# Kernel optimization log

Measured on AMD Instinct MI355X. Metric: run time of the kernel, lower is better.

## Reference

```python
import jax, jax.numpy as jnp
import numpy as np

B, N, DIM = 8, 1024, 1024
HEADS, DIM_HEAD = 16, 64
INNER = HEADS * DIM_HEAD  # 1024


def setup_inputs() -> dict:
    key = jax.random.key(0)
    k1, k2, k3 = jax.random.split(key, 3)
    x = jax.random.normal(k1, (B, N, DIM), dtype=jnp.float32)
    # Dense kernels (Glorot-ish scale for numerical sanity)
    w_qkv = jax.random.normal(k2, (DIM, 3 * INNER), dtype=jnp.float32) * (DIM ** -0.5)
    w_out = jax.random.normal(k3, (INNER, DIM), dtype=jnp.float32) * (INNER ** -0.5)
    b_out = jnp.zeros((DIM,), dtype=jnp.float32)
    return {"x": x, "w_qkv": w_qkv, "w_out": w_out, "b_out": b_out}


def reference(x, w_qkv, w_out, b_out):
    scale = DIM_HEAD ** -0.5
    qkv = x @ w_qkv                                   # [B, N, 3*INNER]
    q, k, v = jnp.split(qkv, 3, axis=-1)              # each [B, N, INNER]

    def to_heads(t):
        # [B, N, H*Dh] -> [B, H, N, Dh]
        return t.reshape(B, N, HEADS, DIM_HEAD).transpose(0, 2, 1, 3)

    q, k, v = to_heads(q), to_heads(k), to_heads(v)
    dots = jnp.einsum("bhid,bhjd->bhij", q, k) * scale   # [B, H, N, N]
    attn = jax.nn.softmax(dots, axis=-1)
    out = jnp.einsum("bhij,bhjd->bhid", attn, v)          # [B, H, N, Dh]
    out = out.transpose(0, 2, 1, 3).reshape(B, N, INNER)  # merge heads
    return out @ w_out + b_out                            # project_out (dropout inactive at inference)
```

## Files before the change

kernel.cpp:

```cpp
#include <hip/hip_runtime.h>
#include <hip/hip_bf16.h>
#include <math.h>

typedef __bf16 bf16_t;
typedef __bf16 bf16x4 __attribute__((ext_vector_type(4)));
typedef __bf16 bf16x8 __attribute__((ext_vector_type(8)));
typedef float f32x4 __attribute__((ext_vector_type(4)));

#define LOG2E 1.44269504088896340736f

__global__ __launch_bounds__(256) void transpose_f32_bf16(const float* __restrict__ in,
                                                          bf16_t* __restrict__ out,
                                                          int R, int C) {
  __shared__ bf16_t t[64][65];
  const int c0 = blockIdx.x * 64, r0 = blockIdx.y * 64;
  const int tx = threadIdx.x, ty = threadIdx.y;
#pragma unroll
  for (int i = 0; i < 16; i++) {
    int r = ty + i * 4;
    t[r][tx] = (bf16_t)in[(size_t)(r0 + r) * C + c0 + tx];
  }
  __syncthreads();
#pragma unroll
  for (int i = 0; i < 16; i++) {
    int r = ty + i * 4;
    out[(size_t)(c0 + r) * R + r0 + tx] = t[tx][r];
  }
}

template <int MODE>
__global__ __launch_bounds__(256) void gemm128(const float* __restrict__ Af,
                                               const bf16_t* __restrict__ Ab,
                                               const bf16_t* __restrict__ Bt,
                                               bf16_t* __restrict__ Qb,
                                               bf16_t* __restrict__ Kb,
                                               bf16_t* __restrict__ Vtb,
                                               const float* __restrict__ bias,
                                               float* __restrict__ Out) {
  constexpr int K = 1024;
  __shared__ __align__(16) bf16_t As[128 * 72];
  __shared__ __align__(16) bf16_t Bs[128 * 72];
  const int m0 = blockIdx.y * 128, n0 = blockIdx.x * 128;
  const int tid = threadIdx.x;
  const int w = tid >> 6, l = tid & 63;
  const int lr = l & 15, lq = l >> 4;
  const int wm = (w & 1) * 64, wn = (w >> 1) * 64;
  f32x4 acc[4][4] = {};

  for (int k0 = 0; k0 < K; k0 += 64) {
    if (MODE == 0) {
#pragma unroll
      for (int i = 0; i < 8; i++) {
        int c = tid + i * 256;
        int r = c >> 4, kc = c & 15;
        f32x4 a = *(const f32x4*)&Af[(size_t)(m0 + r) * K + k0 + kc * 4];
        bf16x4 v;
        v[0] = (bf16_t)a[0]; v[1] = (bf16_t)a[1];
        v[2] = (bf16_t)a[2]; v[3] = (bf16_t)a[3];
        *(bf16x4*)&As[r * 72 + kc * 4] = v;
      }
    } else {
#pragma unroll
      for (int i = 0; i < 4; i++) {
        int c = tid + i * 256;
        int r = c >> 3, kc = c & 7;
        *(bf16x8*)&As[r * 72 + kc * 8] =
            *(const bf16x8*)&Ab[(size_t)(m0 + r) * K + k0 + kc * 8];
      }
    }
#pragma unroll
    for (int i = 0; i < 4; i++) {
      int c = tid + i * 256;
      int r = c >> 3, kc = c & 7;
      *(bf16x8*)&Bs[r * 72 + kc * 8] =
          *(const bf16x8*)&Bt[(size_t)(n0 + r) * K + k0 + kc * 8];
    }
    __syncthreads();
#pragma unroll
    for (int ks = 0; ks < 2; ks++) {
      bf16x8 af[4], bfr[4];
#pragma unroll
      for (int mt = 0; mt < 4; mt++)
        af[mt] = *(const bf16x8*)&As[(wm + mt * 16 + lr) * 72 + ks * 32 + lq * 8];
#pragma unroll
      for (int nt = 0; nt < 4; nt++)
        bfr[nt] = *(const bf16x8*)&Bs[(wn + nt * 16 + lr) * 72 + ks * 32 + lq * 8];
#pragma unroll
      for (int mt = 0; mt < 4; mt++)
#pragma unroll
        for (int nt = 0; nt < 4; nt++)
          acc[mt][nt] = __builtin_amdgcn_mfma_f32_16x16x32_bf16(af[mt], bfr[nt],
                                                                acc[mt][nt], 0, 0, 0);
    }
    __syncthreads();
  }

#pragma unroll
  for (int mt = 0; mt < 4; mt++)
#pragma unroll
    for (int nt = 0; nt < 4; nt++)
#pragma unroll
      for (int i = 0; i < 4; i++) {
        int m = m0 + wm + mt * 16 + lq * 4 + i;
        int c = n0 + wn + nt * 16 + lr;
        float v = acc[mt][nt][i];
        if (MODE == 1) {
          Out[(size_t)m * 1024 + c] = v + bias[c];
        } else {
          int b = m >> 10, n = m & 1023;
          int which = c >> 10, cc = c & 1023;
          int hh = cc >> 6, d = cc & 63;
          size_t qk = ((size_t)((b * 16 + hh) * 1024 + n)) * 64 + d;
          if (which == 0)
            Qb[qk] = (bf16_t)(v * (0.125f * LOG2E));
          else if (which == 1)
            Kb[qk] = (bf16_t)v;
          else
            Vtb[((size_t)((b * 16 + hh) * 64 + d)) * 1024 + n] = (bf16_t)v;
        }
      }
}

#define KVS 68
#define PS  72
__global__ __launch_bounds__(256) void attn128(const bf16_t* __restrict__ Qb,
                                               const bf16_t* __restrict__ Kb,
                                               const bf16_t* __restrict__ Vtb,
                                               bf16_t* __restrict__ Ob) {
  __shared__ __align__(16) bf16_t Ks[2][64 * KVS];
  __shared__ __align__(16) bf16_t Vs[2][64 * KVS];
  __shared__ __align__(16) bf16_t Pl[4 * 32 * PS];
  const int bid = blockIdx.x;
  const int qt = bid & 7, h = (bid >> 3) & 15, b = bid >> 7;
  const bf16_t* Qh = Qb + (size_t)((b * 16 + h) * 1024) * 64;
  const bf16_t* Kh = Kb + (size_t)((b * 16 + h) * 1024) * 64;
  const bf16_t* Vh = Vtb + (size_t)((b * 16 + h) * 64) * 1024;
  const int tid = threadIdx.x, w = tid >> 6, l = tid & 63;
  const int lr = l & 15, lq = l >> 4;
  const int q0 = qt * 128 + w * 32;

  bf16x8 onesf;
#pragma unroll
  for (int i = 0; i < 8; i++) onesf[i] = (lr == 0) ? (bf16_t)1.0f : (bf16_t)0.0f;

  const int sr = tid >> 3, sc = tid & 7;

  bf16x8 qf[2][2];
#pragma unroll
  for (int mt = 0; mt < 2; mt++)
#pragma unroll
    for (int ks = 0; ks < 2; ks++)
      qf[mt][ks] = *(const bf16x8*)&Qh[(size_t)(q0 + mt * 16 + lr) * 64 + ks * 32 + lq * 8];

  {
    bf16x8 k0 = *(const bf16x8*)&Kh[(size_t)sr * 64 + sc * 8];
    bf16x8 k1 = *(const bf16x8*)&Kh[(size_t)(sr + 32) * 64 + sc * 8];
    bf16x8 v0 = *(const bf16x8*)&Vh[(size_t)sr * 1024 + sc * 8];
    bf16x8 v1 = *(const bf16x8*)&Vh[(size_t)(sr + 32) * 1024 + sc * 8];
    *(bf16x8*)&Ks[0][sr * KVS + sc * 8] = k0;
    *(bf16x8*)&Ks[0][(sr + 32) * KVS + sc * 8] = k1;
    *(bf16x8*)&Vs[0][sr * KVS + sc * 8] = v0;
    *(bf16x8*)&Vs[0][(sr + 32) * KVS + sc * 8] = v1;
  }
  __syncthreads();

  f32x4 o[2][4] = {};
  f32x4 o5[2] = {};
  bf16_t* pw = &Pl[w * 32 * PS];

  for (int it = 0; it < 16; ++it) {
    const int buf = it & 1;
    bf16x8 nk0, nk1, nv0, nv1;
    if (it < 15) {
      const int jn = (it + 1) * 64;
      nk0 = *(const bf16x8*)&Kh[(size_t)(jn + sr) * 64 + sc * 8];
      nk1 = *(const bf16x8*)&Kh[(size_t)(jn + sr + 32) * 64 + sc * 8];
      nv0 = *(const bf16x8*)&Vh[(size_t)sr * 1024 + jn + sc * 8];
      nv1 = *(const bf16x8*)&Vh[(size_t)(sr + 32) * 1024 + jn + sc * 8];
    }
    f32x4 s[2][4] = {};
#pragma unroll
    for (int ks = 0; ks < 2; ks++)
#pragma unroll
      for (int nt = 0; nt < 4; nt++) {
        bf16x8 kf = *(const bf16x8*)&Ks[buf][(nt * 16 + lr) * KVS + ks * 32 + lq * 8];
#pragma unroll
        for (int mt = 0; mt < 2; mt++)
          s[mt][nt] = __builtin_amdgcn_mfma_f32_16x16x32_bf16(qf[mt][ks], kf, s[mt][nt], 0, 0, 0);
      }
#pragma unroll
    for (int mt = 0; mt < 2; mt++)
#pragma unroll
      for (int nt = 0; nt < 4; nt++)
#pragma unroll
        for (int i = 0; i < 4; i++)
          pw[(mt * 16 + lq * 4 + i) * PS + nt * 16 + lr] = (bf16_t)exp2f(s[mt][nt][i]);
#pragma unroll
    for (int ks = 0; ks < 2; ks++) {
      bf16x8 af[2];
#pragma unroll
      for (int mt = 0; mt < 2; mt++)
        af[mt] = *(const bf16x8*)&pw[(mt * 16 + lr) * PS + ks * 32 + lq * 8];
#pragma unroll
      for (int nt = 0; nt < 4; nt++) {
        bf16x8 vf = *(const bf16x8*)&Vs[buf][(nt * 16 + lr) * KVS + ks * 32 + lq * 8];
#pragma unroll
        for (int mt = 0; mt < 2; mt++)
          o[mt][nt] = __builtin_amdgcn_mfma_f32_16x16x32_bf16(af[mt], vf, o[mt][nt], 0, 0, 0);
      }
#pragma unroll
      for (int mt = 0; mt < 2; mt++)
        o5[mt] = __builtin_amdgcn_mfma_f32_16x16x32_bf16(af[mt], onesf, o5[mt], 0, 0, 0);
    }
    if (it < 15) {
      *(bf16x8*)&Ks[buf ^ 1][sr * KVS + sc * 8] = nk0;
      *(bf16x8*)&Ks[buf ^ 1][(sr + 32) * KVS + sc * 8] = nk1;
      *(bf16x8*)&Vs[buf ^ 1][sr * KVS + sc * 8] = nv0;
      *(bf16x8*)&Vs[buf ^ 1][(sr + 32) * KVS + sc * 8] = nv1;
    }
    __syncthreads();
  }
#pragma unroll
  for (int mt = 0; mt < 2; mt++)
#pragma unroll
    for (int i = 0; i < 4; i++) {
      float lsum = __shfl(o5[mt][i], lq * 16);
      float inv = 1.0f / lsum;
      int grow = b * 1024 + q0 + mt * 16 + lq * 4 + i;
#pragma unroll
      for (int nt = 0; nt < 4; nt++) {
        int col = h * 64 + nt * 16 + lr;
        Ob[(size_t)grow * 1024 + col] = (bf16_t)(o[mt][nt][i] * inv);
      }
    }
}

extern "C" void kernel_launch(void* const* d_in, const int* in_sizes, int n_in,
                              void* d_out, int out_size, void* d_ws, size_t ws_size,
                              hipStream_t stream) {
  const float* x     = (const float*)d_in[0];
  const float* w_qkv = (const float*)d_in[1];
  const float* w_out = (const float*)d_in[2];
  const float* b_out = (const float*)d_in[3];
  float* out = (float*)d_out;

  bf16_t* ws = (bf16_t*)d_ws;
  const size_t SZ = (size_t)8 * 1024 * 1024;
  bf16_t* Qb  = ws;
  bf16_t* Kb  = Qb + SZ;
  bf16_t* Vtb = Kb + SZ;
  bf16_t* Ob  = Vtb + SZ;
  bf16_t* Wqt = Ob + SZ;
  bf16_t* Wot = Wqt + (size_t)3072 * 1024;

  hipLaunchKernelGGL(transpose_f32_bf16, dim3(48, 16), dim3(64, 4), 0, stream,
                     w_qkv, Wqt, 1024, 3072);
  hipLaunchKernelGGL(transpose_f32_bf16, dim3(16, 16), dim3(64, 4), 0, stream,
                     w_out, Wot, 1024, 1024);
  hipLaunchKernelGGL((gemm128<0>), dim3(24, 64), dim3(256), 0, stream,
                     x, (const bf16_t*)nullptr, Wqt, Qb, Kb, Vtb,
                     (const float*)nullptr, (float*)nullptr);
  hipLaunchKernelGGL(attn128, dim3(1024), dim3(256), 0, stream, Qb, Kb, Vtb, Ob);
  hipLaunchKernelGGL((gemm128<1>), dim3(8, 64), dim3(256), 0, stream,
                     (const float*)nullptr, Ob, Wot, (bf16_t*)nullptr,
                     (bf16_t*)nullptr, (bf16_t*)nullptr, b_out, out);
}
```

Measured before the change: 301.2 us.

## Load GEMM tiles directly into LDS with XOR swizzle; pre-convert x to bf16

The GEMM now uses global_load_lds to move bf16 tiles straight from global memory into shared memory, skipping the register round trip. It replaces the padded 72-stride layout with an XOR-swizzled 64-stride layout to avoid bank conflicts. Because that path needs bf16 input, x is converted to bf16 by a separate kernel into the Ob workspace, which is reused before attention writes it. This adds one extra pass over x and keeps the single-buffered loop with its syncs.

```diff
diff --git a/kernel.cpp b/kernel.cpp
--- a/kernel.cpp
+++ b/kernel.cpp
@@ -8,6 +8,22 @@
 typedef float f32x4 __attribute__((ext_vector_type(4)));
 
 #define LOG2E 1.44269504088896340736f
+
+#define GL2LDS(g, l)                                                     \
+  __builtin_amdgcn_global_load_lds(                                      \
+      (const __attribute__((address_space(1))) unsigned int*)(g),        \
+      (__attribute__((address_space(3))) unsigned int*)(l), 16, 0, 0)
+
+__global__ __launch_bounds__(256) void convert_f32_bf16(const float* __restrict__ in,
+                                                        bf16_t* __restrict__ out) {
+  const size_t idx = (size_t)(blockIdx.x * 256 + threadIdx.x) * 8;
+  f32x4 a = *(const f32x4*)&in[idx];
+  f32x4 b = *(const f32x4*)&in[idx + 4];
+  bf16x8 v;
+#pragma unroll
+  for (int i = 0; i < 4; i++) { v[i] = (bf16_t)a[i]; v[i + 4] = (bf16_t)b[i]; }
+  *(bf16x8*)&out[idx] = v;
+}
 
 __global__ __launch_bounds__(256) void transpose_f32_bf16(const float* __restrict__ in,
                                                           bf16_t* __restrict__ out,
@@ -29,8 +45,7 @@
 }
 
 template <int MODE>
-__global__ __launch_bounds__(256) void gemm128(const float* __restrict__ Af,
-                                               const bf16_t* __restrict__ Ab,
+__global__ __launch_bounds__(256) void gemm128(const bf16_t* __restrict__ A,
                                                const bf16_t* __restrict__ Bt,
                                                bf16_t* __restrict__ Qb,
                                                bf16_t* __restrict__ Kb,
@@ -38,53 +53,40 @@
                                                const float* __restrict__ bias,
                                                float* __restrict__ Out) {
   constexpr int K = 1024;
-  __shared__ __align__(16) bf16_t As[128 * 72];
-  __shared__ __align__(16) bf16_t Bs[128 * 72];
+  __shared__ __align__(16) bf16_t As[128 * 64];
+  __shared__ __align__(16) bf16_t Bs[128 * 64];
   const int m0 = blockIdx.y * 128, n0 = blockIdx.x * 128;
   const int tid = threadIdx.x;
   const int w = tid >> 6, l = tid & 63;
   const int lr = l & 15, lq = l >> 4;
+  const int lrx = lr & 7;
   const int wm = (w & 1) * 64, wn = (w >> 1) * 64;
+  const int sR[4] = {(0 * 256 + tid) >> 3, (1 * 256 + tid) >> 3,
+                     (2 * 256 + tid) >> 3, (3 * 256 + tid) >> 3};
+  int sC[4];
+#pragma unroll
+  for (int i = 0; i < 4; i++) sC[i] = ((tid & 7) ^ (sR[i] & 7)) * 8;
   f32x4 acc[4][4] = {};
 
   for (int k0 = 0; k0 < K; k0 += 64) {
-    if (MODE == 0) {
-#pragma unroll
-      for (int i = 0; i < 8; i++) {
-        int c = tid + i * 256;
-        int r = c >> 4, kc = c & 15;
-        f32x4 a = *(const f32x4*)&Af[(size_t)(m0 + r) * K + k0 + kc * 4];
-        bf16x4 v;
-        v[0] = (bf16_t)a[0]; v[1] = (bf16_t)a[1];
-        v[2] = (bf16_t)a[2]; v[3] = (bf16_t)a[3];
-        *(bf16x4*)&As[r * 72 + kc * 4] = v;
-      }
-    } else {
-#pragma unroll
-      for (int i = 0; i < 4; i++) {
-        int c = tid + i * 256;
-        int r = c >> 3, kc = c & 7;
-        *(bf16x8*)&As[r * 72 + kc * 8] =
-            *(const bf16x8*)&Ab[(size_t)(m0 + r) * K + k0 + kc * 8];
-      }
-    }
 #pragma unroll
     for (int i = 0; i < 4; i++) {
-      int c = tid + i * 256;
-      int r = c >> 3, kc = c & 7;
-      *(bf16x8*)&Bs[r * 72 + kc * 8] =
-          *(const bf16x8*)&Bt[(size_t)(n0 + r) * K + k0 + kc * 8];
+      const int ldsoff = (i * 256 + w * 64) * 8;
+      GL2LDS(&A[(size_t)(m0 + sR[i]) * K + k0 + sC[i]], &As[ldsoff]);
+      GL2LDS(&Bt[(size_t)(n0 + sR[i]) * K + k0 + sC[i]], &Bs[ldsoff]);
     }
     __syncthreads();
 #pragma unroll
     for (int ks = 0; ks < 2; ks++) {
+      const int g = ks * 4 + lq;
+      const int sw = ((g ^ lrx) << 3);
       bf16x8 af[4], bfr[4];
 #pragma unroll
       for (int mt = 0; mt < 4; mt++)
-        af[mt] = *(const bf16x8*)&As[(wm + mt * 16 + lr) * 72 + ks * 32 + lq * 8];
+        af[mt] = *(const bf16x8*)&As[((wm + mt * 16 + lr) << 6) + sw];
 #pragma unroll
       for (int nt = 0; nt < 4; nt++)
-        bfr[nt] = *(const bf16x8*)&Bs[(wn + nt * 16 + lr) * 72 + ks * 32 + lq * 8];
+        bfr[nt] = *(const bf16x8*)&Bs[((wn + nt * 16 + lr) << 6) + sw];
 #pragma unroll
       for (int mt = 0; mt < 4; mt++)
 #pragma unroll
@@ -252,16 +254,17 @@
   bf16_t* Ob  = Vtb + SZ;
   bf16_t* Wqt = Ob + SZ;
   bf16_t* Wot = Wqt + (size_t)3072 * 1024;
-
+  bf16_t* Xb  = Ob;
+
+  hipLaunchKernelGGL(convert_f32_bf16, dim3(4096), dim3(256), 0, stream, x, Xb);
   hipLaunchKernelGGL(transpose_f32_bf16, dim3(48, 16), dim3(64, 4), 0, stream,
                      w_qkv, Wqt, 1024, 3072);
   hipLaunchKernelGGL(transpose_f32_bf16, dim3(16, 16), dim3(64, 4), 0, stream,
                      w_out, Wot, 1024, 1024);
   hipLaunchKernelGGL((gemm128<0>), dim3(24, 64), dim3(256), 0, stream,
-                     x, (const bf16_t*)nullptr, Wqt, Qb, Kb, Vtb,
-                     (const float*)nullptr, (float*)nullptr);
+                     Xb, Wqt, Qb, Kb, Vtb, (const float*)nullptr, (float*)nullptr);
   hipLaunchKernelGGL(attn128, dim3(1024), dim3(256), 0, stream, Qb, Kb, Vtb, Ob);
   hipLaunchKernelGGL((gemm128<1>), dim3(8, 64), dim3(256), 0, stream,
-                     (const float*)nullptr, Ob, Wot, (bf16_t*)nullptr,
-                     (bf16_t*)nullptr, (bf16_t*)nullptr, b_out, out);
-}
+                     Ob, Wot, (bf16_t*)nullptr, (bf16_t*)nullptr, (bf16_t*)nullptr,
+                     b_out, out);
+}
```

After: 282.2 us. 6.3% less time.
